# Optimization experiments

Hardware: AMD Instinct MI355X
Metric: run time of the kernel (lower is better)

The kernel has to match this reference:

```python
import jax, jax.numpy as jnp
import numpy as np

N, C_IN, C_OUT, C_REL, T, V = 64, 256, 256, 32, 64, 25

def conv1x1(x, w, b):
    # x: (n, ci, a, b), w: (co, ci), b: (co,) -> (n, co, a, b)
    return jnp.einsum('oc,ncab->noab', w, x) + b[None, :, None, None]

def setup_inputs() -> dict:
    key = jax.random.key(0)
    ks = jax.random.split(key, 10)
    s_in = 1.0 / np.sqrt(C_IN)
    s_rel = 1.0 / np.sqrt(C_REL)
    return {
        'x': jax.random.normal(ks[0], (N, C_IN, T, V), dtype=jnp.float32),
        'A': jax.random.normal(ks[1], (V, V), dtype=jnp.float32),
        'w1': jax.random.uniform(ks[2], (C_REL, C_IN), jnp.float32, -s_in, s_in),
        'b1': jax.random.uniform(ks[3], (C_REL,), jnp.float32, -s_in, s_in),
        'w2': jax.random.uniform(ks[4], (C_REL, C_IN), jnp.float32, -s_in, s_in),
        'b2': jax.random.uniform(ks[5], (C_REL,), jnp.float32, -s_in, s_in),
        'w3': jax.random.uniform(ks[6], (C_OUT, C_IN), jnp.float32, -s_in, s_in),
        'b3': jax.random.uniform(ks[7], (C_OUT,), jnp.float32, -s_in, s_in),
        'w4': jax.random.uniform(ks[8], (C_OUT, C_REL), jnp.float32, -s_rel, s_rel),
        'b4': jax.random.uniform(ks[9], (C_OUT,), jnp.float32, -s_rel, s_rel),
        'threhold': 0,
        'alpha': 1,
    }

def reference(x, A, w1, b1, w2, b2, w3, b3, w4, b4, threhold, alpha):
    # x: (n, c, t, v)
    # pooled 1x1 convs: fold the T-mean before the channel mix (linear ops commute)
    xm = x.mean(-2)                                   # (n, c, v)
    x1 = jnp.einsum('oc,ncv->nov', w1, xm) + b1[None, :, None]   # (n, r, v)
    x2 = jnp.einsum('oc,ncv->nov', w2, xm) + b2[None, :, None]   # (n, r, v)
    x3 = conv1x1(x, w3, b3)                           # (n, co, t, v)
    # channel-wise affinity: outer difference + tanh -> (n, r, v, v)
    aff = jnp.tanh(x1[:, :, :, None] - x2[:, :, None, :])
    # 1x1 conv over rel channels, scale, add adjacency
    attn = jnp.einsum('or,nruv->nouv', w4, aff) + b4[None, :, None, None]
    attn = attn * alpha + A[None, None]               # (n, co, v, v)
    # graph conv contraction
    out = jnp.einsum('ncuv,nctu->nctv', attn, x3)     # (n, co, t, v)
    return out
```

## Files before the change

kernel.cpp:

```cpp
#include <hip/hip_runtime.h>

#define N_  64
#define CI  256
#define CO  256
#define CR  32
#define T_  64
#define V_  25
#define TV  (T_*V_)
#define VV  (V_*V_)
#define ATS 640

typedef __attribute__((ext_vector_type(8))) short bshort8;
typedef __attribute__((ext_vector_type(4))) short bshort4;
typedef __attribute__((ext_vector_type(4))) float f32x4;

__device__ inline unsigned short f2bf(float f) {
    unsigned int u = __float_as_uint(f);
    return (unsigned short)((u + 0x7FFFu + ((u >> 16) & 1u)) >> 16);
}

__global__ __launch_bounds__(256) void k_cvt_w3f(const float* __restrict__ w3,
                                                 unsigned short* __restrict__ w3f) {
    int f = blockIdx.x * 256 + threadIdx.x;
    int lane = f & 63;
    int ks = (f >> 6) & 7;
    int ot = f >> 9;
    const float* src = w3 + (size_t)(ot * 16 + (lane & 15)) * CI + ks * 32 + (lane >> 4) * 8;
    bshort8 v;
    #pragma unroll
    for (int i = 0; i < 8; ++i) v[i] = (short)f2bf(src[i]);
    *(bshort8*)(w3f + (size_t)f * 8) = v;
}

__global__ __launch_bounds__(256) void k_cvt_w4f(const float* __restrict__ w4,
                                                 unsigned short* __restrict__ w4f) {
    int f = blockIdx.x * 256 + threadIdx.x;
    int lane = f & 63;
    int ot = f >> 6;
    const float* src = w4 + (size_t)(ot * 16 + (lane & 15)) * CR + (lane >> 4) * 8;
    bshort8 v;
    #pragma unroll
    for (int i = 0; i < 8; ++i) v[i] = (short)f2bf(src[i]);
    *(bshort8*)(w4f + (size_t)f * 8) = v;
}

__global__ __launch_bounds__(256) void k_mean(const float* __restrict__ x,
                                              float* __restrict__ xm) {
    int idx = blockIdx.x * 256 + threadIdx.x;
    if (idx >= N_ * CI * V_) return;
    int v  = idx % V_;
    int nc = idx / V_;
    const float* p = x + (size_t)nc * TV + v;
    float s = 0.f;
    for (int t = 0; t < T_; ++t) s += p[t * V_];
    xm[idx] = s * (1.f / T_);
}

__global__ __launch_bounds__(256) void k_xpose(const float* __restrict__ x,
                                               unsigned short* __restrict__ xT) {
    int n  = blockIdx.x;
    int c0 = blockIdx.y * 64;
    int j0 = blockIdx.z * 64;
    __shared__ float L[64 * 65];
    int tid = threadIdx.x;
    #pragma unroll
    for (int p = 0; p < 4; ++p) {
        int cc = p * 16 + (tid >> 4);
        int f4 = tid & 15;
        float4 v = *(const float4*)(x + (size_t)n * CI * TV + (size_t)(c0 + cc) * TV + j0 + f4 * 4);
        L[(f4 * 4 + 0) * 65 + cc] = v.x;
        L[(f4 * 4 + 1) * 65 + cc] = v.y;
        L[(f4 * 4 + 2) * 65 + cc] = v.z;
        L[(f4 * 4 + 3) * 65 + cc] = v.w;
    }
    __syncthreads();
    int jl = tid >> 2, seg = tid & 3;
    bshort8 o0v, o1v;
    #pragma unroll
    for (int q = 0; q < 8; ++q) o0v[q] = (short)f2bf(L[jl * 65 + seg * 16 + q]);
    #pragma unroll
    for (int q = 0; q < 8; ++q) o1v[q] = (short)f2bf(L[jl * 65 + seg * 16 + 8 + q]);
    unsigned short* dst = xT + (size_t)n * (TV * CI) + (size_t)(j0 + jl) * CI + c0 + seg * 16;
    *(bshort8*)dst = o0v;
    *(bshort8*)(dst + 8) = o1v;
}

__global__ __launch_bounds__(256) void k_x1x2(const float* __restrict__ xm,
                                              const float* __restrict__ w1,
                                              const float* __restrict__ b1,
                                              const float* __restrict__ w2,
                                              const float* __restrict__ b2,
                                              float* __restrict__ x1,
                                              float* __restrict__ x2) {
    int n = blockIdx.x;
    __shared__ float s_xm[CI * V_];
    const float4* src = (const float4*)(xm + (size_t)n * CI * V_);
    for (int i = threadIdx.x; i < CI * V_ / 4; i += 256) ((float4*)s_xm)[i] = src[i];
    __syncthreads();
    for (int idx = threadIdx.x; idx < CR * V_; idx += 256) {
        int r = idx / V_, v = idx % V_;
        float a1 = 0.f, a2 = 0.f;
        for (int c = 0; c < CI; ++c) {
            float xv = s_xm[c * V_ + v];
            a1 += w1[r * CI + c] * xv;
            a2 += w2[r * CI + c] * xv;
        }
        x1[n * CR * V_ + idx] = a1 + b1[r];
        x2[n * CR * V_ + idx] = a2 + b2[r];
    }
}

__global__ __launch_bounds__(256) void k_attn(const float* __restrict__ x1,
                                              const float* __restrict__ x2,
                                              const unsigned short* __restrict__ w4f,
                                              const float* __restrict__ b4,
                                              const float* __restrict__ A,
                                              const int* __restrict__ alpha_p,
                                              unsigned short* __restrict__ attnT) {
    int n = blockIdx.x;
    __shared__ float s_x1[CR * V_];
    __shared__ float s_x2[CR * V_];
    __shared__ float s_A[VV];
    int tid = threadIdx.x;
    float alpha = (float)alpha_p[0];
    for (int i = tid; i < CR * V_; i += 256) {
        s_x1[i] = x1[n * CR * V_ + i];
        s_x2[i] = x2[n * CR * V_ + i];
    }
    for (int i = tid; i < VV; i += 256) s_A[i] = A[i];
    __syncthreads();
    int wave = tid >> 6, lane = tid & 63;
    int task = blockIdx.y * 4 + wave;
    int og   = task & 3;
    int ug   = task >> 2;
    int o0   = og * 64;
    int quad = lane >> 4, c16 = lane & 15;
    bshort8 a[4];
    #pragma unroll
    for (int ot = 0; ot < 4; ++ot)
        a[ot] = *(const bshort8*)(w4f + (size_t)(((og * 4) + ot) * 64 + lane) * 8);
    float4 bv[4];
    #pragma unroll
    for (int ot = 0; ot < 4; ++ot)
        bv[ot] = *(const float4*)(b4 + o0 + ot * 16 + quad * 4);
    int r0 = quad * 8;
    #pragma unroll
    for (int it = 0; it < 5; ++it) {
        int uv0 = (ug * 5 + it) * 16;
        int uvc = uv0 + c16;
        bool valid = uvc < VV;
        int uvcc = valid ? uvc : (VV - 1);
        int u = uvcc % V_, v = uvcc / V_;
        bshort8 b;
        #pragma unroll
        for (int i = 0; i < 8; ++i) {
            float d = s_x1[(r0 + i) * V_ + u] - s_x2[(r0 + i) * V_ + v];
            b[i] = (short)f2bf(tanhf(d));
        }
        float Auv = s_A[u * V_ + v];
        f32x4 acc[4];
        #pragma unroll
        for (int ot = 0; ot < 4; ++ot)
            acc[ot] = __builtin_amdgcn_mfma_f32_16x16x32_bf16(a[ot], b, (f32x4){0,0,0,0}, 0, 0, 0);
        if (valid) {
            #pragma unroll
            for (int ot = 0; ot < 4; ++ot) {
                #pragma unroll
                for (int r = 0; r < 4; ++r) {
                    int o = o0 + ot * 16 + quad * 4 + r;
                    float bval = (r == 0) ? bv[ot].x : (r == 1) ? bv[ot].y
                               : (r == 2) ? bv[ot].z : bv[ot].w;
                    attnT[(size_t)(n * CO + o) * ATS + uvc] =
                        f2bf((acc[ot][r] + bval) * alpha + Auv);
                }
            }
        }
    }
}

__global__ __launch_bounds__(256) void k_gemm1(const unsigned short* __restrict__ xT,
                                               const unsigned short* __restrict__ w3f,
                                               const float* __restrict__ b3,
                                               unsigned short* __restrict__ x3) {
    int n = blockIdx.x, j0 = blockIdx.y * 64;
    __shared__ unsigned short sB[64 * 256];
    int tid  = threadIdx.x;
    int lane = tid & 63, wave = tid >> 6;
    const unsigned short* gB = xT + (size_t)n * (TV * CI) + (size_t)j0 * CI;
    #pragma unroll
    for (int pp = 0; pp < 8; ++pp) {
        int task = pp * 256 + tid;
        int row = task >> 5, part = task & 31;
        int phys = part ^ (row & 7);
        *(bshort8*)(&sB[row * 256 + phys * 8]) = *(const bshort8*)(gB + row * 256 + part * 8);
    }
    __syncthreads();
    int quad = lane >> 4, c16 = lane & 15;
    const bshort8* Af = (const bshort8*)w3f;
    f32x4 acc[4][4];
    #pragma unroll
    for (int mt = 0; mt < 4; ++mt)
        #pragma unroll
        for (int nt = 0; nt < 4; ++nt) acc[mt][nt] = (f32x4){0,0,0,0};
    #pragma unroll
    for (int ks = 0; ks < 8; ++ks) {
        bshort8 b[4], a[4];
        #pragma unroll
        for (int nt = 0; nt < 4; ++nt) {
            int rB = nt * 16 + c16;
            int cidx = ks * 4 + quad;
            b[nt] = *(const bshort8*)(&sB[rB * 256 + ((cidx ^ (rB & 7)) << 3)]);
        }
        #pragma unroll
        for (int mt = 0; mt < 4; ++mt)
            a[mt] = Af[(size_t)(((wave * 4 + mt) * 8 + ks) * 64) + lane];
        #pragma unroll
        for (int mt = 0; mt < 4; ++mt)
            #pragma unroll
            for (int nt = 0; nt < 4; ++nt)
                acc[mt][nt] = __builtin_amdgcn_mfma_f32_16x16x32_bf16(a[mt], b[nt], acc[mt][nt], 0, 0, 0);
    }
    __syncthreads();
    unsigned short* eS = sB;
    #pragma unroll
    for (int pass = 0; pass < 2; ++pass) {
        if ((wave >> 1) == pass) {
            #pragma unroll
            for (int mt = 0; mt < 4; ++mt) {
                int o = wave * 64 + mt * 16 + quad * 4;
                float4 bvv = *(const float4*)(b3 + o);
                int ol = (wave & 1) * 64 + mt * 16 + quad * 4;
                #pragma unroll
                for (int nt = 0; nt < 4; ++nt) {
                    int jc = nt * 16 + c16;
                    eS[(ol + 0) * 72 + jc] = f2bf(acc[mt][nt][0] + bvv.x);
                    eS[(ol + 1) * 72 + jc] = f2bf(acc[mt][nt][1] + bvv.y);
                    eS[(ol + 2) * 72 + jc] = f2bf(acc[mt][nt][2] + bvv.z);
                    eS[(ol + 3) * 72 + jc] = f2bf(acc[mt][nt][3] + bvv.w);
                }
            }
        }
        __syncthreads();
        #pragma unroll
        for (int i = 0; i < 4; ++i) {
            int task = i * 256 + tid;
            int orow = task >> 3, seg = task & 7;
            bshort8 vv = *(const bshort8*)&eS[orow * 72 + seg * 8];
            *(bshort8*)(x3 + (size_t)(n * CO + pass * 128 + orow) * TV + j0 + seg * 8) = vv;
        }
        __syncthreads();
    }
}

__global__ __launch_bounds__(256) void k_contract(const unsigned short* __restrict__ x3,
                                                  const unsigned short* __restrict__ attnT,
                                                  float* __restrict__ out) {
    int no0 = blockIdx.x * 4;
    __shared__ __align__(16) unsigned char smem[28672];
    unsigned short* sA = (unsigned short*)smem;
    unsigned short* sB = (unsigned short*)(smem + 16384);
    float*          sO = (float*)smem;
    int tid = threadIdx.x;
    #pragma unroll
    for (int i = 0; i < 7; ++i) {
        int task = i * 256 + tid;
        if (task < 1792) {
            int p = task / 448, rem = task % 448;
            sA[p * 2048 + (rem / 7) * 32 + 25 + rem % 7] = 0;
        }
    }
    {
        int task = tid;
        for (int i = 0; i < 3; ++i, task += 256)
            if (task < 700) {
                int p = task / 175, rem = task % 175;
                sB[p * 1024 + (rem / 7) * 32 + 25 + rem % 7] = 0;
            }
    }
    #pragma unroll
    for (int i = 0; i < 4; ++i) {
        int task = i * 256 + tid;
        if (task < 800) {
            int p = task / 200, e8 = task % 200;
            bshort8 vv = *(const bshort8*)(x3 + (size_t)(no0 + p) * TV + e8 * 8);
            #pragma unroll
            for (int k = 0; k < 8; ++k) {
                int j = e8 * 8 + k;
                int t = j / 25, u = j % 25;
                sA[p * 2048 + t * 32 + u] = (unsigned short)vv[k];
            }
        }
    }
    #pragma unroll
    for (int i = 0; i < 2; ++i) {
        int task = i * 256 + tid;
        if (task < 316) {
            int p = task / 79, e8 = task % 79;
            bshort8 vv = *(const bshort8*)(attnT + (size_t)(no0 + p) * ATS + e8 * 8);
            #pragma unroll
            for (int k = 0; k < 8; ++k) {
                int idx = e8 * 8 + k;
                if (idx < VV) {
                    int v = idx / 25, u = idx % 25;
                    sB[p * 1024 + v * 32 + u] = (unsigned short)vv[k];
                }
            }
        }
    }
    __syncthreads();
    int p = tid >> 6, lane = tid & 63;
    int quad = lane >> 4, c16 = lane & 15;
    const unsigned short* pA = sA + p * 2048;
    const unsigned short* pB = sB + p * 1024;
    bshort8 a[4], b[2];
    #pragma unroll
    for (int mt = 0; mt < 4; ++mt) a[mt] = *(const bshort8*)&pA[(mt * 16 + c16) * 32 + quad * 8];
    #pragma unroll
    for (int nt = 0; nt < 2; ++nt) b[nt] = *(const bshort8*)&pB[(nt * 16 + c16) * 32 + quad * 8];
    f32x4 acc[4][2];
    #pragma unroll
    for (int mt = 0; mt < 4; ++mt)
        #pragma unroll
        for (int nt = 0; nt < 2; ++nt)
            acc[mt][nt] = __builtin_amdgcn_mfma_f32_16x16x32_bf16(a[mt], b[nt], (f32x4){0,0,0,0}, 0, 0, 0);
    __syncthreads();
    float* pO = sO + p * 1792;
    #pragma unroll
    for (int mt = 0; mt < 4; ++mt)
        #pragma unroll
        for (int nt = 0; nt < 2; ++nt) {
            int v = nt * 16 + c16;
            if (v < V_) {
                #pragma unroll
                for (int r = 0; r < 4; ++r) {
                    int t = mt * 16 + quad * 4 + r;
                    pO[t * 28 + v] = acc[mt][nt][r];
                }
            }
        }
    __syncthreads();
    #pragma unroll
    for (int i = 0; i < 25; ++i) {
        int idx = i * 256 + tid;
        int p2 = idx / TV, rem = idx % TV;
        int t = rem / 25, v = rem % 25;
        out[(size_t)(no0 + p2) * TV + rem] = sO[p2 * 1792 + t * 28 + v];
    }
}

extern "C" void kernel_launch(void* const* d_in, const int* in_sizes, int n_in,
                              void* d_out, int out_size, void* d_ws, size_t ws_size,
                              hipStream_t stream) {
    const float* x  = (const float*)d_in[0];
    const float* A  = (const float*)d_in[1];
    const float* w1 = (const float*)d_in[2];
    const float* b1 = (const float*)d_in[3];
    const float* w2 = (const float*)d_in[4];
    const float* b2 = (const float*)d_in[5];
    const float* w3 = (const float*)d_in[6];
    const float* b3 = (const float*)d_in[7];
    const float* w4 = (const float*)d_in[8];
    const float* b4 = (const float*)d_in[9];
    const int* alpha_p = (const int*)d_in[11];
    float* out = (float*)d_out;

    float* ws = (float*)d_ws;
    float* xm = ws;
    float* x1 = ws + 409600;
    float* x2 = ws + 460800;
    unsigned short* attnT = (unsigned short*)(ws + 512000);
    unsigned short* w3f   = attnT + (size_t)16384 * ATS;
    unsigned short* xT    = w3f + 65536;
    unsigned short* x3    = xT + (size_t)26214400;
    unsigned short* w4f   = x3 + (size_t)26214400;

    k_cvt_w3f<<<32, 256, 0, stream>>>(w3, w3f);
    k_cvt_w4f<<<4, 256, 0, stream>>>(w4, w4f);
    k_xpose<<<dim3(N_, 4, 25), 256, 0, stream>>>(x, xT);
    k_mean<<<(N_ * CI * V_ + 255) / 256, 256, 0, stream>>>(x, xm);
    k_x1x2<<<N_, 256, 0, stream>>>(xm, w1, b1, w2, b2, x1, x2);
    k_attn<<<dim3(N_, 8), 256, 0, stream>>>(x1, x2, w4f, b4, A, alpha_p, attnT);
    k_gemm1<<<dim3(N_, 25), 256, 0, stream>>>(xT, w3f, b3, x3);
    k_contract<<<4096, 256, 0, stream>>>(x3, attnT, out);
}
```

Measured before the change: 354.3 us.

## Fuse x transpose and bf16 conversion into GEMM load; merge weight-convert kernels

Removes the separate transpose kernel that wrote a bf16 transposed copy of x to global memory. The GEMM now reads fp32 x directly, converts it to bf16 and scatters it transposed into shared memory under a new XOR swizzle. This drops a full write and reread of the large intermediate, at the cost of scalar 16-bit LDS stores and more conversion work inside the GEMM. The two weight-conversion kernels are also merged into one launch.

```diff
diff --git a/kernel.cpp b/kernel.cpp
--- a/kernel.cpp
+++ b/kernel.cpp
@@ -11,7 +11,6 @@
 #define ATS 640
 
 typedef __attribute__((ext_vector_type(8))) short bshort8;
-typedef __attribute__((ext_vector_type(4))) short bshort4;
 typedef __attribute__((ext_vector_type(4))) float f32x4;
 
 __device__ inline unsigned short f2bf(float f) {
@@ -19,29 +18,31 @@
     return (unsigned short)((u + 0x7FFFu + ((u >> 16) & 1u)) >> 16);
 }
 
-__global__ __launch_bounds__(256) void k_cvt_w3f(const float* __restrict__ w3,
-                                                 unsigned short* __restrict__ w3f) {
-    int f = blockIdx.x * 256 + threadIdx.x;
-    int lane = f & 63;
-    int ks = (f >> 6) & 7;
-    int ot = f >> 9;
-    const float* src = w3 + (size_t)(ot * 16 + (lane & 15)) * CI + ks * 32 + (lane >> 4) * 8;
-    bshort8 v;
-    #pragma unroll
-    for (int i = 0; i < 8; ++i) v[i] = (short)f2bf(src[i]);
-    *(bshort8*)(w3f + (size_t)f * 8) = v;
-}
-
-__global__ __launch_bounds__(256) void k_cvt_w4f(const float* __restrict__ w4,
-                                                 unsigned short* __restrict__ w4f) {
-    int f = blockIdx.x * 256 + threadIdx.x;
-    int lane = f & 63;
-    int ot = f >> 6;
-    const float* src = w4 + (size_t)(ot * 16 + (lane & 15)) * CR + (lane >> 4) * 8;
-    bshort8 v;
-    #pragma unroll
-    for (int i = 0; i < 8; ++i) v[i] = (short)f2bf(src[i]);
-    *(bshort8*)(w4f + (size_t)f * 8) = v;
+__global__ __launch_bounds__(256) void k_cvt_w(const float* __restrict__ w3,
+                                               const float* __restrict__ w4,
+                                               unsigned short* __restrict__ w3f,
+                                               unsigned short* __restrict__ w4f) {
+    int b = blockIdx.x;
+    if (b < 32) {
+        int f = b * 256 + threadIdx.x;
+        int lane = f & 63;
+        int ks = (f >> 6) & 7;
+        int ot = f >> 9;
+        const float* src = w3 + (size_t)(ot * 16 + (lane & 15)) * CI + ks * 32 + (lane >> 4) * 8;
+        bshort8 v;
+        #pragma unroll
+        for (int i = 0; i < 8; ++i) v[i] = (short)f2bf(src[i]);
+        *(bshort8*)(w3f + (size_t)f * 8) = v;
+    } else {
+        int f = (b - 32) * 256 + threadIdx.x;
+        int lane = f & 63;
+        int ot = f >> 6;
+        const float* src = w4 + (size_t)(ot * 16 + (lane & 15)) * CR + (lane >> 4) * 8;
+        bshort8 v;
+        #pragma unroll
+        for (int i = 0; i < 8; ++i) v[i] = (short)f2bf(src[i]);
+        *(bshort8*)(w4f + (size_t)f * 8) = v;
+    }
 }
 
 __global__ __launch_bounds__(256) void k_mean(const float* __restrict__ x,
@@ -54,35 +55,6 @@
     float s = 0.f;
     for (int t = 0; t < T_; ++t) s += p[t * V_];
     xm[idx] = s * (1.f / T_);
-}
-
-__global__ __launch_bounds__(256) void k_xpose(const float* __restrict__ x,
-                                               unsigned short* __restrict__ xT) {
-    int n  = blockIdx.x;
-    int c0 = blockIdx.y * 64;
-    int j0 = blockIdx.z * 64;
-    __shared__ float L[64 * 65];
-    int tid = threadIdx.x;
-    #pragma unroll
-    for (int p = 0; p < 4; ++p) {
-        int cc = p * 16 + (tid >> 4);
-        int f4 = tid & 15;
-        float4 v = *(const float4*)(x + (size_t)n * CI * TV + (size_t)(c0 + cc) * TV + j0 + f4 * 4);
-        L[(f4 * 4 + 0) * 65 + cc] = v.x;
-        L[(f4 * 4 + 1) * 65 + cc] = v.y;
-        L[(f4 * 4 + 2) * 65 + cc] = v.z;
-        L[(f4 * 4 + 3) * 65 + cc] = v.w;
-    }
-    __syncthreads();
-    int jl = tid >> 2, seg = tid & 3;
-    bshort8 o0v, o1v;
-    #pragma unroll
-    for (int q = 0; q < 8; ++q) o0v[q] = (short)f2bf(L[jl * 65 + seg * 16 + q]);
-    #pragma unroll
-    for (int q = 0; q < 8; ++q) o1v[q] = (short)f2bf(L[jl * 65 + seg * 16 + 8 + q]);
-    unsigned short* dst = xT + (size_t)n * (TV * CI) + (size_t)(j0 + jl) * CI + c0 + seg * 16;
-    *(bshort8*)dst = o0v;
-    *(bshort8*)(dst + 8) = o1v;
 }
 
 __global__ __launch_bounds__(256) void k_x1x2(const float* __restrict__ xm,
@@ -178,7 +150,7 @@
     }
 }
 
-__global__ __launch_bounds__(256) void k_gemm1(const unsigned short* __restrict__ xT,
+__global__ __launch_bounds__(256) void k_gemm1(const float* __restrict__ x,
                                                const unsigned short* __restrict__ w3f,
                                                const float* __restrict__ b3,
                                                unsigned short* __restrict__ x3) {
@@ -186,13 +158,19 @@
     __shared__ unsigned short sB[64 * 256];
     int tid  = threadIdx.x;
     int lane = tid & 63, wave = tid >> 6;
-    const unsigned short* gB = xT + (size_t)n * (TV * CI) + (size_t)j0 * CI;
-    #pragma unroll
-    for (int pp = 0; pp < 8; ++pp) {
-        int task = pp * 256 + tid;
-        int row = task >> 5, part = task & 31;
-        int phys = part ^ (row & 7);
-        *(bshort8*)(&sB[row * 256 + phys * 8]) = *(const bshort8*)(gB + row * 256 + part * 8);
+    const float* gx = x + (size_t)n * CI * TV + j0;
+    for (int i = 0; i < 16; ++i) {
+        int task = i * 256 + tid;
+        int c = task >> 4, chunk = task & 15;
+        float4 v = *(const float4*)(gx + (size_t)c * TV + chunk * 4);
+        int g0 = c >> 3, cl = c & 7;
+        #pragma unroll
+        for (int k = 0; k < 4; ++k) {
+            int j = chunk * 4 + k;
+            int f = g0 ^ (j & 7) ^ ((j >> 2) & 7);
+            float val = (k == 0) ? v.x : (k == 1) ? v.y : (k == 2) ? v.z : v.w;
+            sB[j * 256 + f * 8 + cl] = f2bf(val);
+        }
     }
     __syncthreads();
     int quad = lane >> 4, c16 = lane & 15;
@@ -209,7 +187,8 @@
         for (int nt = 0; nt < 4; ++nt) {
             int rB = nt * 16 + c16;
             int cidx = ks * 4 + quad;
-            b[nt] = *(const bshort8*)(&sB[rB * 256 + ((cidx ^ (rB & 7)) << 3)]);
+            int f = cidx ^ (rB & 7) ^ ((rB >> 2) & 7);
+            b[nt] = *(const bshort8*)(&sB[rB * 256 + f * 8]);
         }
         #pragma unroll
         for (int mt = 0; mt < 4; ++mt)
@@ -370,16 +349,13 @@
     float* x2 = ws + 460800;
     unsigned short* attnT = (unsigned short*)(ws + 512000);
     unsigned short* w3f   = attnT + (size_t)16384 * ATS;
-    unsigned short* xT    = w3f + 65536;
-    unsigned short* x3    = xT + (size_t)26214400;
-    unsigned short* w4f   = x3 + (size_t)26214400;
-
-    k_cvt_w3f<<<32, 256, 0, stream>>>(w3, w3f);
-    k_cvt_w4f<<<4, 256, 0, stream>>>(w4, w4f);
-    k_xpose<<<dim3(N_, 4, 25), 256, 0, stream>>>(x, xT);
+    unsigned short* w4f   = w3f + 65536;
+    unsigned short* x3    = w4f + 16384;
+
+    k_cvt_w<<<36, 256, 0, stream>>>(w3, w4, w3f, w4f);
     k_mean<<<(N_ * CI * V_ + 255) / 256, 256, 0, stream>>>(x, xm);
     k_x1x2<<<N_, 256, 0, stream>>>(xm, w1, b1, w2, b2, x1, x2);
     k_attn<<<dim3(N_, 8), 256, 0, stream>>>(x1, x2, w4f, b4, A, alpha_p, attnT);
-    k_gemm1<<<dim3(N_, 25), 256, 0, stream>>>(xT, w3f, b3, x3);
+    k_gemm1<<<dim3(N_, 25), 256, 0, stream>>>(x, w3f, b3, x3);
     k_contract<<<4096, 256, 0, stream>>>(x3, attnT, out);
 }
```

Result: faster. 323.2 us (-8.8%).
